# Optimization experiments

Measured on AMD Instinct MI355X. Metric: run time of the kernel, lower is better.

Reference implementation:

```python
import jax, jax.numpy as jnp
import numpy as np

ALPHA = 0.4
EPS = float(np.finfo(np.float32).eps)  # torch.finfo(fp32).eps
BATCH, VOCAB, RANK = 256, 128000, 64


def setup_inputs() -> dict:
    key = jax.random.key(0)
    k1, k2, k3 = jax.random.split(key, 3)
    token_ids = jax.random.randint(k1, (BATCH, 1), 0, VOCAB, dtype=jnp.int64 if jax.config.jax_enable_x64 else jnp.int32)
    logits = jax.random.normal(k2, (BATCH, VOCAB), dtype=jnp.float32)
    W = jax.random.normal(k3, (VOCAB, RANK), dtype=jnp.float32)
    return {"token_ids": token_ids, "logits": logits, "W": W}


def reference(token_ids, logits, W):
    # _rescaled_mint_no_cast (remove_basis=True):
    #   Lp_raw = L @ W @ W.T - L   (low-rank mint, basis removed)
    Lp_raw = (logits @ W) @ W.T - logits  # [B, V]
    # Guarantee max|L'| <= max|L| via global abs-max rescale.
    scale = jnp.max(jnp.abs(logits)) / jnp.maximum(jnp.max(jnp.abs(Lp_raw)), EPS)
    minted = Lp_raw * scale
    # Modes.Lerp: torch.lerp(minted, logits, alpha) = minted + alpha*(logits - minted)
    return minted + ALPHA * (logits - minted)
```

## Files before the change

kernel.cpp:

```cpp
#include <hip/hip_runtime.h>
#include <math.h>

#define ALPHA_F 0.4f
#define FP32_EPS 1.1920928955078125e-7f
#define NB 256
#define NV 128000
#define NR 64

typedef _Float16 half_t;
typedef _Float16 half2_t __attribute__((ext_vector_type(2)));
typedef _Float16 half4_t __attribute__((ext_vector_type(4)));
typedef _Float16 half8 __attribute__((ext_vector_type(8)));
typedef float f32x4 __attribute__((ext_vector_type(4)));


__global__ __launch_bounds__(256, 8) void k0_prep(const float* __restrict__ W,
                                                  half_t* __restrict__ Wg,
                                                  half_t* __restrict__ Wf,
                                                  float* __restrict__ P,
                                                  unsigned* __restrict__ maxbits) {
    __shared__ half_t tile[128 * 72];
    const int t  = threadIdx.x;
    const int k0 = blockIdx.x * 128;

    if (blockIdx.x < 64) P[blockIdx.x * 256 + t] = 0.f;
    if (blockIdx.x == 0 && t < 2) maxbits[t] = 0u;

#pragma unroll
    for (int i = 0; i < 8; ++i) {
        const int f  = i * 256 + t;
        const int kr = f >> 4;
        const int n4 = (f & 15) * 4;
        const float4 v = *(const float4*)(W + (size_t)(k0 + kr) * NR + n4);
        half2_t h01 = { (half_t)v.x, (half_t)v.y };
        half2_t h23 = { (half_t)v.z, (half_t)v.w };
        *(half2_t*)&tile[kr * 72 + n4]     = h01;
        *(half2_t*)&tile[kr * 72 + n4 + 2] = h23;
    }
    __syncthreads();

#pragma unroll
    for (int i = 0; i < 4; ++i) {
        const int idx  = i * 256 + t;
        const int kk_l = idx >> 8;
        const int rem  = idx & 255;
        const int nt   = rem >> 6;
        const int lane = rem & 63;
        const int q = lane >> 4, il = lane & 15;
        half8 v;
#pragma unroll
        for (int j = 0; j < 8; ++j)
            v[j] = tile[(kk_l * 32 + q * 8 + j) * 72 + nt * 16 + il];
        const int kt = blockIdx.x * 4 + kk_l;
        *(half8*)(Wg + ((size_t)(kt * 4 + nt) * 64 + lane) * 8) = v;
    }

    if (Wf) {
#pragma unroll
        for (int i = 0; i < 4; ++i) {
            const int idx  = i * 256 + t;
            const int vt_l = idx >> 7;
            const int ks   = (idx >> 6) & 1;
            const int lane = idx & 63;
            const int q = lane >> 4, il = lane & 15;
            half8 v = *(const half8*)&tile[(vt_l * 16 + il) * 72 + ks * 32 + q * 8];
            const int vt = blockIdx.x * 8 + vt_l;
            *(half8*)(Wf + ((size_t)(vt * 2 + ks) * 64 + lane) * 8) = v;
        }
    }
}

__global__ __launch_bounds__(256, 4) void k1_pmm(const float* __restrict__ L,
                                                 const half_t* __restrict__ Wg,
                                                 float* __restrict__ Ppart,
                                                 half_t* __restrict__ Lh,
                                                 unsigned* __restrict__ maxbits) {
    __shared__ char lds[64 * 512];
    __shared__ float red[4];
    const int t  = threadIdx.x;
    const int l  = t & 63;
    const int w  = t >> 6;
    const int q  = l >> 4;
    const int il = l & 15;
    const int chunk = blockIdx.x;
    const int mq    = blockIdx.y;
    const int row0  = mq * 64;
    const int col0  = chunk * 256;

    float amax = 0.f;

    {
        const int tr = t >> 5;
        const int tc = t & 31;
        float4 fv[16];
#pragma unroll
        for (int p = 0; p < 8; ++p) {
            const int r = p * 8 + tr;
            const float* lp = L + (size_t)(row0 + r) * NV + col0 + tc * 8;
            fv[2 * p]     = *(const float4*)lp;
            fv[2 * p + 1] = *(const float4*)(lp + 4);
        }
#pragma unroll
        for (int p = 0; p < 8; ++p) {
            const int r = p * 8 + tr;
            const float4 f0 = fv[2 * p], f1 = fv[2 * p + 1];
            amax = fmaxf(amax, fmaxf(fmaxf(fabsf(f0.x), fabsf(f0.y)),
                                     fmaxf(fabsf(f0.z), fabsf(f0.w))));
            amax = fmaxf(amax, fmaxf(fmaxf(fabsf(f1.x), fabsf(f1.y)),
                                     fmaxf(fabsf(f1.z), fabsf(f1.w))));
            half8 h = { (half_t)f0.x, (half_t)f0.y, (half_t)f0.z, (half_t)f0.w,
                        (half_t)f1.x, (half_t)f1.y, (half_t)f1.z, (half_t)f1.w };
            if (Lh) *(half8*)(Lh + (size_t)(row0 + r) * NV + col0 + tc * 8) = h;
            const int off = r * 512 + ((tc * 16) ^ (tr << 4));
            *(half8*)(lds + off) = h;
        }
    }
    __syncthreads();

    f32x4 acc[4] = {};
    const int arow = w * 16 + il;
    const int abase = arow * 512;
    const int axor  = (il & 7) << 4;

#define K1_LOADB(dst, kss) do {                                                  \
    const half_t* wp_ = Wg + ((size_t)((chunk * 8 + (kss)) * 4) * 64 + l) * 8;   \
    dst[0] = *(const half8*)(wp_);                                               \
    dst[1] = *(const half8*)(wp_ + 64 * 8);                                      \
    dst[2] = *(const half8*)(wp_ + 2 * 64 * 8);                                  \
    dst[3] = *(const half8*)(wp_ + 3 * 64 * 8); } while (0)

#define K1_MFMA(bv, kss) do {                                                    \
    const half8 a_ = *(const half8*)(lds + ((abase + (kss) * 64 + q * 16) ^ axor)); \
    acc[0] = __builtin_amdgcn_mfma_f32_16x16x32_f16(a_, bv[0], acc[0], 0, 0, 0); \
    acc[1] = __builtin_amdgcn_mfma_f32_16x16x32_f16(a_, bv[1], acc[1], 0, 0, 0); \
    acc[2] = __builtin_amdgcn_mfma_f32_16x16x32_f16(a_, bv[2], acc[2], 0, 0, 0); \
    acc[3] = __builtin_amdgcn_mfma_f32_16x16x32_f16(a_, bv[3], acc[3], 0, 0, 0); } while (0)

    half8 ba[4], bb[4];
    K1_LOADB(ba, 0);
#pragma unroll
    for (int ks = 0; ks < 8; ks += 2) {
        K1_LOADB(bb, ks + 1);
        K1_MFMA(ba, ks);
        if (ks + 2 < 8) K1_LOADB(ba, ks + 2);
        K1_MFMA(bb, ks + 1);
    }

    float* pb = Ppart + (size_t)(chunk * 4 + mq) * 4096;
#pragma unroll
    for (int nt = 0; nt < 4; ++nt)
#pragma unroll
        for (int i = 0; i < 4; ++i)
            pb[(w * 16 + q * 4 + i) * 64 + nt * 16 + il] = acc[nt][i];

#pragma unroll
    for (int off = 32; off > 0; off >>= 1)
        amax = fmaxf(amax, __shfl_xor(amax, off, 64));
    if (l == 0) red[w] = amax;
    __syncthreads();
    if (threadIdx.x == 0) {
        float m = fmaxf(fmaxf(red[0], red[1]), fmaxf(red[2], red[3]));
        atomicMax(&maxbits[0], __float_as_uint(m));
    }
}

__global__ __launch_bounds__(256) void k1b_reduce(const float* __restrict__ Ppart,
                                                  float* __restrict__ P) {
    const int g  = blockIdx.x * 256 + threadIdx.x;
    const int M  = g >> 6, n = g & 63;
    const int mq = M >> 6, r = M & 63;
    const float* p = Ppart + ((size_t)(blockIdx.y * 25) * 4 + mq) * 4096 + r * 64 + n;
    float s = 0.f;
#pragma unroll 5
    for (int c = 0; c < 25; ++c) s += p[(size_t)c * 4 * 4096];
    atomicAdd(&P[g], s);
}

template <bool FAST, bool IS_OUT>
__global__ __launch_bounds__(256, 8) void k23(const float* __restrict__ L,
                                              const half_t* __restrict__ Lh,
                                              const float* __restrict__ W,
                                              const half_t* __restrict__ Wf,
                                              const float* __restrict__ P,
                                              unsigned* __restrict__ maxbits,
                                              float* __restrict__ out) {
    __shared__ float T[32 * 132];
    __shared__ float red[4];
    const int l  = threadIdx.x & 63;
    const int w  = threadIdx.x >> 6;
    const int q  = l >> 4;
    const int il = l & 15;
    const int nc = blockIdx.x;
    const int mq = blockIdx.y;

    half8 a[2][2];
#pragma unroll
    for (int mt = 0; mt < 2; ++mt)
#pragma unroll
        for (int ks = 0; ks < 2; ++ks) {
            const float* pp = P + (size_t)(mq * 32 + mt * 16 + il) * NR + ks * 32 + q * 8;
            const float4 f0 = *(const float4*)pp;
            const float4 f1 = *(const float4*)(pp + 4);
            a[mt][ks] = { (half_t)f0.x, (half_t)f0.y, (half_t)f0.z, (half_t)f0.w,
                          (half_t)f1.x, (half_t)f1.y, (half_t)f1.z, (half_t)f1.w };
        }
#pragma unroll
    for (int ntl = 0; ntl < 2; ++ntl) {
        const int vt = nc * 8 + w * 2 + ntl;
        half8 b[2];
        if (FAST) {
#pragma unroll
            for (int ks = 0; ks < 2; ++ks)
                b[ks] = *(const half8*)(Wf + ((size_t)(vt * 2 + ks) * 64 + l) * 8);
        } else {
#pragma unroll
            for (int ks = 0; ks < 2; ++ks) {
                const float* wp = W + (size_t)(vt * 16 + il) * NR + ks * 32 + q * 8;
                const float4 f0 = *(const float4*)wp;
                const float4 f1 = *(const float4*)(wp + 4);
                b[ks] = { (half_t)f0.x, (half_t)f0.y, (half_t)f0.z, (half_t)f0.w,
                          (half_t)f1.x, (half_t)f1.y, (half_t)f1.z, (half_t)f1.w };
            }
        }
#pragma unroll
        for (int mt = 0; mt < 2; ++mt) {
            f32x4 acc = {};
            acc = __builtin_amdgcn_mfma_f32_16x16x32_f16(a[mt][0], b[0], acc, 0, 0, 0);
            acc = __builtin_amdgcn_mfma_f32_16x16x32_f16(a[mt][1], b[1], acc, 0, 0, 0);
#pragma unroll
            for (int i = 0; i < 4; ++i)
                T[(mt * 16 + q * 4 + i) * 132 + w * 32 + ntl * 16 + il] = acc[i];
        }
    }
    __syncthreads();

    float c1 = 0.f, mx = 0.f;
    if (IS_OUT) {
        const float maxL  = __uint_as_float(maxbits[0]);
        const float maxLp = fmaxf(__uint_as_float(maxbits[1]), FP32_EPS);
        c1 = (1.f - ALPHA_F) * (maxL / maxLp);
    }
#pragma unroll
    for (int i = 0; i < 4; ++i) {
        const int e = i * 1024 + threadIdx.x * 4;
        const int r = e >> 7, c = e & 127;
        const size_t gaddr = (size_t)(mq * 32 + r) * NV + nc * 128 + c;
        const float4 tv = *(const float4*)&T[r * 132 + c];
        float4 lv;
        if (FAST) {
            const half4_t lh = *(const half4_t*)(Lh + gaddr);
            lv = make_float4((float)lh[0], (float)lh[1], (float)lh[2], (float)lh[3]);
        } else {
            lv = *(const float4*)(L + gaddr);
        }
        if (IS_OUT) {
            float4 o;
            o.x = fmaf(c1, tv.x - lv.x, ALPHA_F * lv.x);
            o.y = fmaf(c1, tv.y - lv.y, ALPHA_F * lv.y);
            o.z = fmaf(c1, tv.z - lv.z, ALPHA_F * lv.z);
            o.w = fmaf(c1, tv.w - lv.w, ALPHA_F * lv.w);
            *(float4*)(out + gaddr) = o;
        } else {
            mx = fmaxf(mx, fmaxf(fmaxf(fabsf(tv.x - lv.x), fabsf(tv.y - lv.y)),
                                 fmaxf(fabsf(tv.z - lv.z), fabsf(tv.w - lv.w))));
        }
    }
    if (!IS_OUT) {
#pragma unroll
        for (int off = 32; off > 0; off >>= 1)
            mx = fmaxf(mx, __shfl_xor(mx, off, 64));
        if (l == 0) red[w] = mx;
        __syncthreads();
        if (threadIdx.x == 0) {
            float m = fmaxf(fmaxf(red[0], red[1]), fmaxf(red[2], red[3]));
            atomicMax(&maxbits[1], __float_as_uint(m));
        }
    }
}

extern "C" void kernel_launch(void* const* d_in, const int* in_sizes, int n_in,
                              void* d_out, int out_size, void* d_ws, size_t ws_size,
                              hipStream_t stream) {
    const float* L = (const float*)d_in[1];
    const float* W = (const float*)d_in[2];
    float* out = (float*)d_out;

    unsigned* maxbits = (unsigned*)d_ws;
    float*    P       = (float*)((char*)d_ws + 256);

    const bool fast = ws_size >= (size_t)140 * 1024 * 1024;
    float* Ppart; half_t* Wg; half_t* Wf; half_t* Lh;
    char* ws = (char*)d_ws;
    if (fast) {
        Ppart = (float*)(ws + ((size_t)1  << 20));
        Wg    = (half_t*)(ws + ((size_t)34 << 20));
        Wf    = (half_t*)(ws + ((size_t)51 << 20));
        Lh    = (half_t*)(ws + ((size_t)68 << 20));
    } else {
        Ppart = (float*)d_out;
        Wg    = (half_t*)((char*)d_out + ((size_t)33 << 20));
        Wf    = nullptr;
        Lh    = nullptr;
    }

    k0_prep   <<<1000,          256, 0, stream>>>(W, Wg, Wf, P, maxbits);
    k1_pmm    <<<dim3(500, 4),  256, 0, stream>>>(L, Wg, Ppart, Lh, maxbits);
    k1b_reduce<<<dim3(64, 20),  256, 0, stream>>>(Ppart, P);
    if (fast) {
        k23<true,  false><<<dim3(1000, 8), 256, 0, stream>>>(L, Lh, W, Wf, P, maxbits, out);
        k23<true,  true ><<<dim3(1000, 8), 256, 0, stream>>>(L, Lh, W, Wf, P, maxbits, out);
    } else {
        k23<false, false><<<dim3(1000, 8), 256, 0, stream>>>(L, Lh, W, Wf, P, maxbits, out);
        k23<false, true ><<<dim3(1000, 8), 256, 0, stream>>>(L, Lh, W, Wf, P, maxbits, out);
    }
}
```

Baseline: 412.4 us.

## Retile projection GEMM to 32-row blocks and split max/output kernels with larger max tile

The first projection kernel now processes 32 rows per block with waves split across rows and N-halves, doubling grid size and allowing higher occupancy (launch bounds 8). The partial-sum layout and reduction kernel are adjusted to match. The max pass becomes a dedicated kernel covering 64 rows per block, so each W tile is reused across more rows and logits loads are batched up front for more memory-level parallelism. The output pass keeps the 32-row tiling. The trade-off is more LDS and registers in the max kernel, which may lower its occupancy.

```diff
diff --git a/kernel.cpp b/kernel.cpp
--- a/kernel.cpp
+++ b/kernel.cpp
@@ -70,12 +70,12 @@
     }
 }
 
-__global__ __launch_bounds__(256, 4) void k1_pmm(const float* __restrict__ L,
+__global__ __launch_bounds__(256, 8) void k1_pmm(const float* __restrict__ L,
                                                  const half_t* __restrict__ Wg,
                                                  float* __restrict__ Ppart,
                                                  half_t* __restrict__ Lh,
                                                  unsigned* __restrict__ maxbits) {
-    __shared__ char lds[64 * 512];
+    __shared__ char lds[32 * 512];
     __shared__ float red[4];
     const int t  = threadIdx.x;
     const int l  = t & 63;
@@ -83,8 +83,8 @@
     const int q  = l >> 4;
     const int il = l & 15;
     const int chunk = blockIdx.x;
-    const int mq    = blockIdx.y;
-    const int row0  = mq * 64;
+    const int mb    = blockIdx.y;
+    const int row0  = mb * 32;
     const int col0  = chunk * 256;
 
     float amax = 0.f;
@@ -92,18 +92,12 @@
     {
         const int tr = t >> 5;
         const int tc = t & 31;
-        float4 fv[16];
-#pragma unroll
-        for (int p = 0; p < 8; ++p) {
+#pragma unroll
+        for (int p = 0; p < 4; ++p) {
             const int r = p * 8 + tr;
             const float* lp = L + (size_t)(row0 + r) * NV + col0 + tc * 8;
-            fv[2 * p]     = *(const float4*)lp;
-            fv[2 * p + 1] = *(const float4*)(lp + 4);
-        }
-#pragma unroll
-        for (int p = 0; p < 8; ++p) {
-            const int r = p * 8 + tr;
-            const float4 f0 = fv[2 * p], f1 = fv[2 * p + 1];
+            const float4 f0 = *(const float4*)lp;
+            const float4 f1 = *(const float4*)(lp + 4);
             amax = fmaxf(amax, fmaxf(fmaxf(fabsf(f0.x), fabsf(f0.y)),
                                      fmaxf(fabsf(f0.z), fabsf(f0.w))));
             amax = fmaxf(amax, fmaxf(fmaxf(fabsf(f1.x), fabsf(f1.y)),
@@ -117,26 +111,23 @@
     }
     __syncthreads();
 
-    f32x4 acc[4] = {};
-    const int arow = w * 16 + il;
+    f32x4 acc[2] = {};
+    const int wr = w & 1, wn = w >> 1;
+    const int arow  = wr * 16 + il;
     const int abase = arow * 512;
     const int axor  = (il & 7) << 4;
 
-#define K1_LOADB(dst, kss) do {                                                  \
-    const half_t* wp_ = Wg + ((size_t)((chunk * 8 + (kss)) * 4) * 64 + l) * 8;   \
-    dst[0] = *(const half8*)(wp_);                                               \
-    dst[1] = *(const half8*)(wp_ + 64 * 8);                                      \
-    dst[2] = *(const half8*)(wp_ + 2 * 64 * 8);                                  \
-    dst[3] = *(const half8*)(wp_ + 3 * 64 * 8); } while (0)
-
-#define K1_MFMA(bv, kss) do {                                                    \
-    const half8 a_ = *(const half8*)(lds + ((abase + (kss) * 64 + q * 16) ^ axor)); \
-    acc[0] = __builtin_amdgcn_mfma_f32_16x16x32_f16(a_, bv[0], acc[0], 0, 0, 0); \
-    acc[1] = __builtin_amdgcn_mfma_f32_16x16x32_f16(a_, bv[1], acc[1], 0, 0, 0); \
-    acc[2] = __builtin_amdgcn_mfma_f32_16x16x32_f16(a_, bv[2], acc[2], 0, 0, 0); \
-    acc[3] = __builtin_amdgcn_mfma_f32_16x16x32_f16(a_, bv[3], acc[3], 0, 0, 0); } while (0)
-
-    half8 ba[4], bb[4];
+#define K1_LOADB(dst, kss) do {                                                      \
+    const half_t* wp_ = Wg + ((size_t)((chunk * 8 + (kss)) * 4 + wn * 2) * 64 + l) * 8; \
+    dst[0] = *(const half8*)(wp_);                                                   \
+    dst[1] = *(const half8*)(wp_ + 64 * 8); } while (0)
+
+#define K1_MFMA(bv, kss) do {                                                        \
+    const half8 a_ = *(const half8*)(lds + ((abase + (kss) * 64 + q * 16) ^ axor));  \
+    acc[0] = __builtin_amdgcn_mfma_f32_16x16x32_f16(a_, bv[0], acc[0], 0, 0, 0);     \
+    acc[1] = __builtin_amdgcn_mfma_f32_16x16x32_f16(a_, bv[1], acc[1], 0, 0, 0); } while (0)
+
+    half8 ba[2], bb[2];
     K1_LOADB(ba, 0);
 #pragma unroll
     for (int ks = 0; ks < 8; ks += 2) {
@@ -146,12 +137,12 @@
         K1_MFMA(bb, ks + 1);
     }
 
-    float* pb = Ppart + (size_t)(chunk * 4 + mq) * 4096;
-#pragma unroll
-    for (int nt = 0; nt < 4; ++nt)
+    float* pb = Ppart + (size_t)(chunk * 8 + mb) * 2048;
+#pragma unroll
+    for (int nt = 0; nt < 2; ++nt)
 #pragma unroll
         for (int i = 0; i < 4; ++i)
-            pb[(w * 16 + q * 4 + i) * 64 + nt * 16 + il] = acc[nt][i];
+            pb[(wr * 16 + q * 4 + i) * 64 + (wn * 2 + nt) * 16 + il] = acc[nt][i];
 
 #pragma unroll
     for (int off = 32; off > 0; off >>= 1)
@@ -168,23 +159,22 @@
                                                   float* __restrict__ P) {
     const int g  = blockIdx.x * 256 + threadIdx.x;
     const int M  = g >> 6, n = g & 63;
-    const int mq = M >> 6, r = M & 63;
-    const float* p = Ppart + ((size_t)(blockIdx.y * 25) * 4 + mq) * 4096 + r * 64 + n;
+    const int mb = M >> 5, r = M & 31;
+    const float* p = Ppart + ((size_t)(blockIdx.y * 25) * 8 + mb) * 2048 + r * 64 + n;
     float s = 0.f;
 #pragma unroll 5
-    for (int c = 0; c < 25; ++c) s += p[(size_t)c * 4 * 4096];
+    for (int c = 0; c < 25; ++c) s += p[(size_t)c * 8 * 2048];
     atomicAdd(&P[g], s);
 }
 
-template <bool FAST, bool IS_OUT>
-__global__ __launch_bounds__(256, 8) void k23(const float* __restrict__ L,
-                                              const half_t* __restrict__ Lh,
-                                              const float* __restrict__ W,
-                                              const half_t* __restrict__ Wf,
-                                              const float* __restrict__ P,
-                                              unsigned* __restrict__ maxbits,
-                                              float* __restrict__ out) {
-    __shared__ float T[32 * 132];
+template <bool FAST>
+__global__ __launch_bounds__(256, 4) void k2_max(const float* __restrict__ L,
+                                                 const half_t* __restrict__ Lh,
+                                                 const float* __restrict__ W,
+                                                 const half_t* __restrict__ Wf,
+                                                 const float* __restrict__ P,
+                                                 unsigned* __restrict__ maxbits) {
+    __shared__ float T[64 * 132];
     __shared__ float red[4];
     const int l  = threadIdx.x & 63;
     const int w  = threadIdx.x >> 6;
@@ -193,12 +183,12 @@
     const int nc = blockIdx.x;
     const int mq = blockIdx.y;
 
-    half8 a[2][2];
-#pragma unroll
-    for (int mt = 0; mt < 2; ++mt)
+    half8 a[4][2];
+#pragma unroll
+    for (int mt = 0; mt < 4; ++mt)
 #pragma unroll
         for (int ks = 0; ks < 2; ++ks) {
-            const float* pp = P + (size_t)(mq * 32 + mt * 16 + il) * NR + ks * 32 + q * 8;
+            const float* pp = P + (size_t)(mq * 64 + mt * 16 + il) * NR + ks * 32 + q * 8;
             const float4 f0 = *(const float4*)pp;
             const float4 f1 = *(const float4*)(pp + 4);
             a[mt][ks] = { (half_t)f0.x, (half_t)f0.y, (half_t)f0.z, (half_t)f0.w,
@@ -223,6 +213,97 @@
             }
         }
 #pragma unroll
+        for (int mt = 0; mt < 4; ++mt) {
+            f32x4 acc = {};
+            acc = __builtin_amdgcn_mfma_f32_16x16x32_f16(a[mt][0], b[0], acc, 0, 0, 0);
+            acc = __builtin_amdgcn_mfma_f32_16x16x32_f16(a[mt][1], b[1], acc, 0, 0, 0);
+#pragma unroll
+            for (int i = 0; i < 4; ++i)
+                T[(mt * 16 + q * 4 + i) * 132 + w * 32 + ntl * 16 + il] = acc[i];
+        }
+    }
+    __syncthreads();
+
+    half4_t lhh[8];
+    float4  lff[8];
+#pragma unroll
+    for (int i = 0; i < 8; ++i) {
+        const int e = i * 1024 + threadIdx.x * 4;
+        const int r = e >> 7, c = e & 127;
+        const size_t gaddr = (size_t)(mq * 64 + r) * NV + nc * 128 + c;
+        if (FAST) lhh[i] = *(const half4_t*)(Lh + gaddr);
+        else      lff[i] = *(const float4*)(L + gaddr);
+    }
+    float mx = 0.f;
+#pragma unroll
+    for (int i = 0; i < 8; ++i) {
+        const int e = i * 1024 + threadIdx.x * 4;
+        const int r = e >> 7, c = e & 127;
+        const float4 tv = *(const float4*)&T[r * 132 + c];
+        float4 lv;
+        if (FAST) lv = make_float4((float)lhh[i][0], (float)lhh[i][1],
+                                   (float)lhh[i][2], (float)lhh[i][3]);
+        else      lv = lff[i];
+        mx = fmaxf(mx, fmaxf(fmaxf(fabsf(tv.x - lv.x), fabsf(tv.y - lv.y)),
+                             fmaxf(fabsf(tv.z - lv.z), fabsf(tv.w - lv.w))));
+    }
+#pragma unroll
+    for (int off = 32; off > 0; off >>= 1)
+        mx = fmaxf(mx, __shfl_xor(mx, off, 64));
+    if (l == 0) red[w] = mx;
+    __syncthreads();
+    if (threadIdx.x == 0) {
+        float m = fmaxf(fmaxf(red[0], red[1]), fmaxf(red[2], red[3]));
+        atomicMax(&maxbits[1], __float_as_uint(m));
+    }
+}
+
+template <bool FAST>
+__global__ __launch_bounds__(256, 8) void k3_out(const float* __restrict__ L,
+                                                 const half_t* __restrict__ Lh,
+                                                 const float* __restrict__ W,
+                                                 const half_t* __restrict__ Wf,
+                                                 const float* __restrict__ P,
+                                                 const unsigned* __restrict__ maxbits,
+                                                 float* __restrict__ out) {
+    __shared__ float T[32 * 132];
+    const int l  = threadIdx.x & 63;
+    const int w  = threadIdx.x >> 6;
+    const int q  = l >> 4;
+    const int il = l & 15;
+    const int nc = blockIdx.x;
+    const int mq = blockIdx.y;
+
+    half8 a[2][2];
+#pragma unroll
+    for (int mt = 0; mt < 2; ++mt)
+#pragma unroll
+        for (int ks = 0; ks < 2; ++ks) {
+            const float* pp = P + (size_t)(mq * 32 + mt * 16 + il) * NR + ks * 32 + q * 8;
+            const float4 f0 = *(const float4*)pp;
+            const float4 f1 = *(const float4*)(pp + 4);
+            a[mt][ks] = { (half_t)f0.x, (half_t)f0.y, (half_t)f0.z, (half_t)f0.w,
+                          (half_t)f1.x, (half_t)f1.y, (half_t)f1.z, (half_t)f1.w };
+        }
+#pragma unroll
+    for (int ntl = 0; ntl < 2; ++ntl) {
+        const int vt = nc * 8 + w * 2 + ntl;
+        half8 b[2];
+        if (FAST) {
+#pragma unroll
+            for (int ks = 0; ks < 2; ++ks)
+                b[ks] = *(const half8*)(Wf + ((size_t)(vt * 2 + ks) * 64 + l) * 8);
+        } else {
+#pragma unroll
+            for (int ks = 0; ks < 2; ++ks) {
+                const float* wp = W + (size_t)(vt * 16 + il) * NR + ks * 32 + q * 8;
+                const float4 f0 = *(const float4*)wp;
+                const float4 f1 = *(const float4*)(wp + 4);
+                b[ks] = { (half_t)f0.x, (half_t)f0.y, (half_t)f0.z, (half_t)f0.w,
+                          (half_t)f1.x, (half_t)f1.y, (half_t)f1.z, (half_t)f1.w };
+            }
+        }
+#pragma unroll
         for (int mt = 0; mt < 2; ++mt) {
             f32x4 acc = {};
             acc = __builtin_amdgcn_mfma_f32_16x16x32_f16(a[mt][0], b[0], acc, 0, 0, 0);
@@ -234,12 +315,9 @@
     }
     __syncthreads();
 
-    float c1 = 0.f, mx = 0.f;
-    if (IS_OUT) {
-        const float maxL  = __uint_as_float(maxbits[0]);
-        const float maxLp = fmaxf(__uint_as_float(maxbits[1]), FP32_EPS);
-        c1 = (1.f - ALPHA_F) * (maxL / maxLp);
-    }
+    const float maxL  = __uint_as_float(maxbits[0]);
+    const float maxLp = fmaxf(__uint_as_float(maxbits[1]), FP32_EPS);
+    const float c1 = (1.f - ALPHA_F) * (maxL / maxLp);
 #pragma unroll
     for (int i = 0; i < 4; ++i) {
         const int e = i * 1024 + threadIdx.x * 4;
@@ -253,28 +331,12 @@
         } else {
             lv = *(const float4*)(L + gaddr);
         }
-        if (IS_OUT) {
-            float4 o;
-            o.x = fmaf(c1, tv.x - lv.x, ALPHA_F * lv.x);
-            o.y = fmaf(c1, tv.y - lv.y, ALPHA_F * lv.y);
-            o.z = fmaf(c1, tv.z - lv.z, ALPHA_F * lv.z);
-            o.w = fmaf(c1, tv.w - lv.w, ALPHA_F * lv.w);
-            *(float4*)(out + gaddr) = o;
-        } else {
-            mx = fmaxf(mx, fmaxf(fmaxf(fabsf(tv.x - lv.x), fabsf(tv.y - lv.y)),
-                                 fmaxf(fabsf(tv.z - lv.z), fabsf(tv.w - lv.w))));
-        }
-    }
-    if (!IS_OUT) {
-#pragma unroll
-        for (int off = 32; off > 0; off >>= 1)
-            mx = fmaxf(mx, __shfl_xor(mx, off, 64));
-        if (l == 0) red[w] = mx;
-        __syncthreads();
-        if (threadIdx.x == 0) {
-            float m = fmaxf(fmaxf(red[0], red[1]), fmaxf(red[2], red[3]));
-            atomicMax(&maxbits[1], __float_as_uint(m));
-        }
+        float4 o;
+        o.x = fmaf(c1, tv.x - lv.x, ALPHA_F * lv.x);
+        o.y = fmaf(c1, tv.y - lv.y, ALPHA_F * lv.y);
+        o.z = fmaf(c1, tv.z - lv.z, ALPHA_F * lv.z);
+        o.w = fmaf(c1, tv.w - lv.w, ALPHA_F * lv.w);
+        *(float4*)(out + gaddr) = o;
     }
 }
 
@@ -304,13 +366,13 @@
     }
 
     k0_prep   <<<1000,          256, 0, stream>>>(W, Wg, Wf, P, maxbits);
-    k1_pmm    <<<dim3(500, 4),  256, 0, stream>>>(L, Wg, Ppart, Lh, maxbits);
+    k1_pmm    <<<dim3(500, 8),  256, 0, stream>>>(L, Wg, Ppart, Lh, maxbits);
     k1b_reduce<<<dim3(64, 20),  256, 0, stream>>>(Ppart, P);
     if (fast) {
-        k23<true,  false><<<dim3(1000, 8), 256, 0, stream>>>(L, Lh, W, Wf, P, maxbits, out);
-        k23<true,  true ><<<dim3(1000, 8), 256, 0, stream>>>(L, Lh, W, Wf, P, maxbits, out);
+        k2_max<true ><<<dim3(1000, 4), 256, 0, stream>>>(L, Lh, W, Wf, P, maxbits);
+        k3_out<true ><<<dim3(1000, 8), 256, 0, stream>>>(L, Lh, W, Wf, P, maxbits, out);
     } else {
-        k23<false, false><<<dim3(1000, 8), 256, 0, stream>>>(L, Lh, W, Wf, P, maxbits, out);
-        k23<false, true ><<<dim3(1000, 8), 256, 0, stream>>>(L, Lh, W, Wf, P, maxbits, out);
-    }
-}
+        k2_max<false><<<dim3(1000, 4), 256, 0, stream>>>(L, Lh, W, Wf, P, maxbits);
+        k3_out<false><<<dim3(1000, 8), 256, 0, stream>>>(L, Lh, W, Wf, P, maxbits, out);
+    }
+}
```

After: 376.2 us. -8.8%, faster.
